# Performance work log

Measured on AMD Instinct MI355X. Metric: run time of the kernel, lower is better.

Reference implementation:

```python
import jax, jax.numpy as jnp
import numpy as np
import math

D = 512          # belief_dim
H = 128          # hidden_dim
R = 64           # relation_dim
M = 8192         # max_beliefs
N = 131072       # candidate pairs
INIT_BIAS = math.log(0.4 / 0.6) * -1.0  # = log(1.5) ~ 0.405465


def _linear_params(key, fan_in, fan_out):
    kw, kb = jax.random.split(key)
    bound = 1.0 / math.sqrt(fan_in)
    W = jax.random.uniform(kw, (fan_in, fan_out), minval=-bound, maxval=bound, dtype=jnp.float32)
    b = jax.random.uniform(kb, (fan_out,), minval=-bound, maxval=bound, dtype=jnp.float32)
    return W, b


def setup_inputs() -> dict:
    key = jax.random.key(0)
    ks = jax.random.split(key, 11)
    beliefs = jax.random.normal(ks[0], (M, D), dtype=jnp.float32)
    src_idx = jax.random.randint(ks[1], (N,), 0, M)
    tgt_idx = jax.random.randint(ks[2], (N,), 0, M)
    # proposal_net: 3D -> H -> H//2 -> 1  (last bias = log(1.5))
    pw1, pb1 = _linear_params(ks[3], 3 * D, H)
    pw2, pb2 = _linear_params(ks[4], H, H // 2)
    pw3, _ = _linear_params(ks[5], H // 2, 1)
    pb3 = jnp.full((1,), INIT_BIAS, dtype=jnp.float32)
    # direction_net: 3D -> H//2 -> 1 (sigmoid)
    dw1, db1 = _linear_params(ks[6], 3 * D, H // 2)
    dw2, db2 = _linear_params(ks[7], H // 2, 1)
    # relation_net: 3D -> H -> R
    rw1, rb1 = _linear_params(ks[8], 3 * D, H)
    rw2, rb2 = _linear_params(ks[9], H, R)
    return {
        "beliefs": beliefs, "src_idx": src_idx, "tgt_idx": tgt_idx,
        "pw1": pw1, "pb1": pb1, "pw2": pw2, "pb2": pb2, "pw3": pw3, "pb3": pb3,
        "dw1": dw1, "db1": db1, "dw2": dw2, "db2": db2,
        "rw1": rw1, "rb1": rb1, "rw2": rw2, "rb2": rb2,
    }


def reference(beliefs, src_idx, tgt_idx,
              pw1, pb1, pw2, pb2, pw3, pb3,
              dw1, db1, dw2, db2,
              rw1, rb1, rw2, rb2):
    src = beliefs[src_idx]                       # [N, D] gather
    tgt = beliefs[tgt_idx]                       # [N, D] gather
    feats = jnp.concatenate([src, tgt, jnp.abs(src - tgt)], axis=-1)  # [N, 3D]

    # proposal head -> edge probability
    h = jax.nn.relu(feats @ pw1 + pb1)
    h = jax.nn.relu(h @ pw2 + pb2)
    probs = jax.nn.sigmoid((h @ pw3 + pb3)[:, 0])                     # [N]

    # direction head -> angle in [0, pi/2]
    d = jax.nn.relu(feats @ dw1 + db1)
    directions = jax.nn.sigmoid((d @ dw2 + db2)[:, 0]) * (jnp.pi / 2)  # [N]

    # relation head -> initial relation vectors
    r = jax.nn.relu(feats @ rw1 + rb1)
    relations = r @ rw2 + rb2                                          # [N, R]

    return probs, directions, relations
```

## Files before the change

kernel.cpp:

```cpp
#include <hip/hip_runtime.h>
#include <hip/hip_bf16.h>


#define DD 512
#define K3 1536
#define ROWS 128
#define LDACT 328
#define BUFS 12288
#define BUFS2 16384

typedef short bf16x8 __attribute__((ext_vector_type(8)));
typedef float f32x4 __attribute__((ext_vector_type(4)));

__device__ inline float b2f(short s) {
    union { float f; unsigned u; } v;
    v.u = ((unsigned)(unsigned short)s) << 16;
    return v.f;
}
__device__ inline short f2b(float f) {
    union { float fl; unsigned u; } v;
    v.fl = f;
    unsigned x = v.u;
    unsigned r = x + 0x7fffu + ((x >> 16) & 1u);
    return (short)(r >> 16);
}
__device__ inline short babsdiff(short a, short b) {
    union { float f; unsigned u; } v;
    v.f = b2f(a) - b2f(b);
    return (short)((v.u & 0x7fffffffu) >> 16);
}
__device__ __forceinline__ bf16x8 babs8(bf16x8 s, bf16x8 t) {
    bf16x8 a;
#pragma unroll
    for (int j = 0; j < 8; j++) a[j] = babsdiff(s[j], t[j]);
    return a;
}

__device__ __forceinline__ int sidx32(int seg, int rt, int lane) {
    return ((seg * 8 + rt) * 64 + lane) * 8;
}
__device__ __forceinline__ void writeStage(short* buf, int rtw, int lnw, int kcb,
                                           bf16x8 s0, bf16x8 s1,
                                           bf16x8 t0, bf16x8 t1) {
    bf16x8 a0 = babs8(s0, t0), a1 = babs8(s1, t1);
    int l0 = kcb * 16 + lnw, l1 = l0 + 16;
    *(bf16x8*)&buf[sidx32(0, rtw, l0)] = s0;
    *(bf16x8*)&buf[sidx32(0, rtw, l1)] = s1;
    *(bf16x8*)&buf[sidx32(1, rtw, l0)] = t0;
    *(bf16x8*)&buf[sidx32(1, rtw, l1)] = t1;
    *(bf16x8*)&buf[sidx32(2, rtw, l0)] = a0;
    *(bf16x8*)&buf[sidx32(2, rtw, l1)] = a1;
}
__device__ __forceinline__ void stage_f32(const float* bs, const float* bt,
                                          short* buf, int rtw, int lnw, int kcb) {
#pragma unroll
    for (int c = 0; c < 2; c++) {
        bf16x8 sb, tb, ab;
#pragma unroll
        for (int h = 0; h < 2; h++) {
            float4 s4 = ((const float4*)bs)[c * 2 + h];
            float4 t4 = ((const float4*)bt)[c * 2 + h];
            float ss[4] = {s4.x, s4.y, s4.z, s4.w};
            float tt[4] = {t4.x, t4.y, t4.z, t4.w};
#pragma unroll
            for (int e = 0; e < 4; e++) {
                int j = h * 4 + e;
                sb[j] = f2b(ss[e]);
                tb[j] = f2b(tt[e]);
                ab[j] = f2b(fabsf(ss[e] - tt[e]));
            }
        }
        int l16 = (kcb + c) * 16 + lnw;
        *(bf16x8*)&buf[sidx32(0, rtw, l16)] = sb;
        *(bf16x8*)&buf[sidx32(1, rtw, l16)] = tb;
        *(bf16x8*)&buf[sidx32(2, rtw, l16)] = ab;
    }
}

#define WT_ELEMS (320 * 1536)
#define P2T_OFF WT_ELEMS
#define R2T_OFF (WT_ELEMS + 64 * 128)
#define PREP_TOT (WT_ELEMS + 2 * 64 * 128)
#define BEL_ELEMS (8192 * 512)
#define BEL_OFF PREP_TOT

__global__ void prep_kernel(const float* __restrict__ pw1,
                            const float* __restrict__ dw1,
                            const float* __restrict__ rw1,
                            const float* __restrict__ pw2,
                            const float* __restrict__ rw2,
                            const float* __restrict__ beliefs,
                            short* __restrict__ ws, int total8) {
    int i8 = blockIdx.x * 256 + threadIdx.x;
    if (i8 >= total8) return;
    int i = i8 * 8;
    bf16x8 o;
    if (i < WT_ELEMS) {
        int n = i / K3, k = i - n * K3;
        const float* src;
        int stride, off;
        if (n < 128)      { src = pw1; stride = 128; off = n; }
        else if (n < 192) { src = dw1; stride = 64;  off = n - 128; }
        else              { src = rw1; stride = 128; off = n - 192; }
#pragma unroll
        for (int j = 0; j < 8; j++) o[j] = f2b(src[(k + j) * stride + off]);
    } else if (i < R2T_OFF) {
        int jj = i - P2T_OFF;
        int n = jj >> 7, k = jj & 127;
#pragma unroll
        for (int j = 0; j < 8; j++) o[j] = f2b(pw2[(k + j) * 64 + n]);
    } else if (i < PREP_TOT) {
        int jj = i - R2T_OFF;
        int n = jj >> 7, k = jj & 127;
#pragma unroll
        for (int j = 0; j < 8; j++) o[j] = f2b(rw2[(k + j) * 64 + n]);
    } else {
        const float4* b4 = (const float4*)(beliefs + (i - BEL_OFF));
        float4 x = b4[0], y = b4[1];
        float v[8] = {x.x, x.y, x.z, x.w, y.x, y.y, y.z, y.w};
#pragma unroll
        for (int j = 0; j < 8; j++) o[j] = f2b(v[j]);
    }
    *(bf16x8*)&ws[i] = o;
}

__global__ __launch_bounds__(256) void prep_bst(
    const short* __restrict__ bel16, const short* __restrict__ WT,
    float* __restrict__ Bs, float* __restrict__ Bt) {
    const int tb = blockIdx.x & 1;
    const int r0 = (blockIdx.x >> 1) * 64;
    const int t = threadIdx.x;
    const int w = t >> 6, lane = t & 63, q = lane >> 4, ln = lane & 15;
    float* Bo = tb ? Bt : Bs;
    const int koff = tb ? 512 : 0;

    f32x4 acc[5][4];
#pragma unroll
    for (int ct = 0; ct < 5; ct++)
#pragma unroll
        for (int rt = 0; rt < 4; rt++) acc[ct][rt] = (f32x4)(0.f);

#pragma unroll
    for (int k0 = 0; k0 < 512; k0 += 128)
#pragma unroll
        for (int kk = 0; kk < 4; kk++) {
            bf16x8 bfr[5];
#pragma unroll
            for (int ct = 0; ct < 5; ct++)
                bfr[ct] = *(const bf16x8*)(WT + (size_t)(w * 80 + ct * 16 + ln) * K3 +
                                           koff + k0 + kk * 32 + q * 8);
#pragma unroll
            for (int rt = 0; rt < 4; rt++) {
                bf16x8 af = *(const bf16x8*)(bel16 +
                    (size_t)(r0 + rt * 16 + ln) * DD + k0 + kk * 32 + q * 8);
#pragma unroll
                for (int ct = 0; ct < 5; ct++)
                    acc[ct][rt] = __builtin_amdgcn_mfma_f32_16x16x32_bf16(
                        af, bfr[ct], acc[ct][rt], 0, 0, 0);
            }
        }
#pragma unroll
    for (int ct = 0; ct < 5; ct++)
#pragma unroll
        for (int rt = 0; rt < 4; rt++)
#pragma unroll
            for (int i = 0; i < 4; i++)
                Bo[(size_t)(r0 + rt * 16 + q * 4 + i) * 320 +
                   w * 80 + ct * 16 + ln] = acc[ct][rt][i];
}

__global__ __launch_bounds__(256, 2) void edge_main2(
    const short* __restrict__ bel16,
    const int* __restrict__ src_idx, const int* __restrict__ tgt_idx,
    const float* __restrict__ Bs, const float* __restrict__ Bt,
    const float* __restrict__ pb1, const float* __restrict__ db1,
    const float* __restrict__ rb1,
    const float* __restrict__ pb2, const float* __restrict__ pw3,
    const float* __restrict__ pb3,
    const float* __restrict__ dw2, const float* __restrict__ db2,
    const float* __restrict__ rb2,
    const short* __restrict__ WT, const short* __restrict__ pw2T,
    const short* __restrict__ rw2T,
    float* __restrict__ out, int N)
{
    __shared__ __align__(16) char smem_u[65536];
    __shared__ int sIdxR[ROWS], tIdxR[ROWS];
    short* As = (short*)smem_u;
    short (*acts)[LDACT] = (short (*)[LDACT])smem_u;

    const int t = threadIdx.x;
    const int r0 = blockIdx.x * ROWS;
    const int w = t >> 6, lane = t & 63, q = lane >> 4, ln = lane & 15;

    if (t < ROWS) sIdxR[t] = src_idx[r0 + t];
    else tIdxR[t - ROWS] = tgt_idx[r0 + t - ROWS];
    __syncthreads();

    const int rr = t >> 1, kh = t & 1;
    const int rtw = rr >> 4, lnw = rr & 15;
    const size_t srow = (size_t)sIdxR[rr] * DD + kh * 64;
    const size_t trow = (size_t)tIdxR[rr] * DD + kh * 64;

    f32x4 acc[5][8];
#pragma unroll
    for (int ct = 0; ct < 5; ct++)
#pragma unroll
        for (int rt = 0; rt < 8; rt++) acc[ct][rt] = (f32x4)(0.f);

#pragma unroll
    for (int c = 0; c < 8; c++) {
        bf16x8 s8 = *(const bf16x8*)(bel16 + srow + c * 8);
        bf16x8 t8 = *(const bf16x8*)(bel16 + trow + c * 8);
        bf16x8 a8 = babs8(s8, t8);
        int gg = kh * 8 + c, kd = gg >> 2, qd = gg & 3;
        *(bf16x8*)&As[((kd * 8 + rtw) * 64 + qd * 16 + lnw) * 8] = a8;
    }
    __syncthreads();

#pragma unroll
    for (int step = 0; step < 4; step++) {
        short* bufC = As + (step & 1) * BUFS2;
        short* bufN = As + ((step & 1) ^ 1) * BUFS2;
        const int k0 = step * 128;
        const bool pf = (step < 3);
        bf16x8 ps0, ps1, pt0, pt1;

#pragma unroll
        for (int kk = 0; kk < 4; kk++) {
            bf16x8 bfr[5];
#pragma unroll
            for (int ct = 0; ct < 5; ct++)
                bfr[ct] = *(const bf16x8*)(WT + (size_t)(w * 80 + ct * 16 + ln) * K3 +
                                           1024 + k0 + kk * 32 + q * 8);
            __builtin_amdgcn_sched_barrier(0);
            if (pf) {
                if (kk > 0) {
                    bf16x8 a0 = babs8(ps0, pt0), a1 = babs8(ps1, pt1);
                    int g0 = kh * 8 + 2 * (kk - 1);
                    int kd0 = g0 >> 2, qd0 = g0 & 3;
                    int g1 = g0 + 1, kd1 = g1 >> 2, qd1 = g1 & 3;
                    *(bf16x8*)&bufN[((kd0 * 8 + rtw) * 64 + qd0 * 16 + lnw) * 8] = a0;
                    *(bf16x8*)&bufN[((kd1 * 8 + rtw) * 64 + qd1 * 16 + lnw) * 8] = a1;
                }
                ps0 = *(const bf16x8*)(bel16 + srow + k0 + 128 + (2 * kk) * 8);
                ps1 = *(const bf16x8*)(bel16 + srow + k0 + 128 + (2 * kk + 1) * 8);
                pt0 = *(const bf16x8*)(bel16 + trow + k0 + 128 + (2 * kk) * 8);
                pt1 = *(const bf16x8*)(bel16 + trow + k0 + 128 + (2 * kk + 1) * 8);
            }
            __builtin_amdgcn_sched_barrier(0);
            __builtin_amdgcn_s_setprio(1);
#pragma unroll
            for (int rt = 0; rt < 8; rt++) {
                bf16x8 af = *(const bf16x8*)&bufC[((kk * 8 + rt) * 64 + lane) * 8];
#pragma unroll
                for (int ct = 0; ct < 5; ct++)
                    acc[ct][rt] = __builtin_amdgcn_mfma_f32_16x16x32_bf16(
                        af, bfr[ct], acc[ct][rt], 0, 0, 0);
            }
            __builtin_amdgcn_s_setprio(0);
        }
        if (pf) {
            bf16x8 a0 = babs8(ps0, pt0), a1 = babs8(ps1, pt1);
            int g0 = kh * 8 + 6;
            int kd0 = g0 >> 2, qd0 = g0 & 3;
            int g1 = g0 + 1, kd1 = g1 >> 2, qd1 = g1 & 3;
            *(bf16x8*)&bufN[((kd0 * 8 + rtw) * 64 + qd0 * 16 + lnw) * 8] = a0;
            *(bf16x8*)&bufN[((kd1 * 8 + rtw) * 64 + qd1 * 16 + lnw) * 8] = a1;
        }
        __syncthreads();
    }

#pragma unroll
    for (int h = 0; h < 2; h++) {
        float bias5[5];
#pragma unroll
        for (int ct = 0; ct < 5; ct++) {
            int col = w * 80 + ct * 16 + ln;
            bias5[ct] = (col < 128) ? pb1[col]
                      : (col < 192) ? db1[col - 128]
                                    : rb1[col - 192];
        }
#pragma unroll
        for (int rt4 = 0; rt4 < 4; rt4++)
#pragma unroll
            for (int i = 0; i < 4; i++) {
                int lrow = rt4 * 16 + q * 4 + i;
                const float* bsp = Bs + (size_t)sIdxR[h * 64 + lrow] * 320 +
                                   w * 80 + ln;
                const float* btp = Bt + (size_t)tIdxR[h * 64 + lrow] * 320 +
                                   w * 80 + ln;
#pragma unroll
                for (int ct = 0; ct < 5; ct++) {
                    float v = acc[ct][h * 4 + rt4][i] +
                              bsp[ct * 16] + btp[ct * 16] + bias5[ct];
                    acts[lrow][w * 80 + ct * 16 + ln] = f2b(fmaxf(v, 0.f));
                }
            }
        __syncthreads();

        {
            f32x4 rc[4];
#pragma unroll
            for (int rt = 0; rt < 4; rt++) rc[rt] = (f32x4)(0.f);
#pragma unroll
            for (int ks = 0; ks < 4; ks++) {
                bf16x8 bfr = *(const bf16x8*)(rw2T + (w * 16 + ln) * 128 +
                                              ks * 32 + q * 8);
#pragma unroll
                for (int rt = 0; rt < 4; rt++) {
                    bf16x8 afr = *(const bf16x8*)&acts[rt * 16 + ln][192 + ks * 32 + q * 8];
                    rc[rt] = __builtin_amdgcn_mfma_f32_16x16x32_bf16(afr, bfr, rc[rt], 0, 0, 0);
                }
            }
            int col = w * 16 + ln;
            float bias = rb2[col];
            float* rel = out + 2 * (size_t)N;
#pragma unroll
            for (int rt = 0; rt < 4; rt++)
#pragma unroll
                for (int i = 0; i < 4; i++) {
                    int grow = r0 + h * 64 + rt * 16 + q * 4 + i;
                    rel[(size_t)grow * 64 + col] = rc[rt][i] + bias;
                }
        }

        f32x4 pc[4];
        {
#pragma unroll
            for (int rt = 0; rt < 4; rt++) pc[rt] = (f32x4)(0.f);
#pragma unroll
            for (int ks = 0; ks < 4; ks++) {
                bf16x8 bfr = *(const bf16x8*)(pw2T + (w * 16 + ln) * 128 +
                                              ks * 32 + q * 8);
#pragma unroll
                for (int rt = 0; rt < 4; rt++) {
                    bf16x8 afr = *(const bf16x8*)&acts[rt * 16 + ln][0 + ks * 32 + q * 8];
                    pc[rt] = __builtin_amdgcn_mfma_f32_16x16x32_bf16(afr, bfr, pc[rt], 0, 0, 0);
                }
            }
        }
        __syncthreads();

        {
            int col = w * 16 + ln;
            float bias = pb2[col];
#pragma unroll
            for (int rt = 0; rt < 4; rt++)
#pragma unroll
                for (int i = 0; i < 4; i++) {
                    int lrow = rt * 16 + q * 4 + i;
                    acts[lrow][col] = f2b(fmaxf(pc[rt][i] + bias, 0.f));
                }
        }
        __syncthreads();

        if (t < 64) {
            float s = pb3[0];
#pragma unroll 8
            for (int k = 0; k < 64; k++) s += b2f(acts[t][k]) * pw3[k];
            float pr = 1.f / (1.f + __expf(-s));
            out[r0 + h * 64 + t] = pr;
        } else if (t < 128) {
            int lrow = t - 64;
            float s = db2[0];
#pragma unroll 8
            for (int k = 0; k < 64; k++) s += b2f(acts[lrow][128 + k]) * dw2[k];
            float dir = (1.f / (1.f + __expf(-s))) * 1.57079632679489662f;
            out[(size_t)N + r0 + h * 64 + lrow] = dir;
        }
        __syncthreads();
    }
}

template<bool BF>
__global__ __launch_bounds__(256, 2) void edge_main(
    const float* __restrict__ beliefs, const short* __restrict__ bel16,
    const int* __restrict__ src_idx, const int* __restrict__ tgt_idx,
    const float* __restrict__ pb1, const float* __restrict__ db1,
    const float* __restrict__ rb1,
    const float* __restrict__ pb2, const float* __restrict__ pw3,
    const float* __restrict__ pb3,
    const float* __restrict__ dw2, const float* __restrict__ db2,
    const float* __restrict__ rb2,
    const short* __restrict__ WT, const short* __restrict__ pw2T,
    const short* __restrict__ rw2T,
    float* __restrict__ out, int N)
{
    __shared__ __align__(16) char smem_u[49152];
    short* As2 = (short*)smem_u;
    short (*acts)[LDACT] = (short (*)[LDACT])smem_u;
    int* sIdx = (int*)smem_u;
    int* tIdx = sIdx + ROWS;

    const int t = threadIdx.x;
    const int r0 = blockIdx.x * ROWS;
    const int w = t >> 6, lane = t & 63, q = lane >> 4, ln = lane & 15;

    if (t < ROWS) sIdx[t] = src_idx[r0 + t] * DD;
    else tIdx[t - ROWS] = tgt_idx[r0 + t - ROWS] * DD;
    __syncthreads();

    const int rrow = t >> 1, kh = t & 1;
    const int rtw = rrow >> 4, lnw = rrow & 15;
    const int kcb = kh * 2;
    const int srow = sIdx[rrow], trow = tIdx[rrow];
    __syncthreads();

    f32x4 acc[5][8];
#pragma unroll
    for (int ct = 0; ct < 5; ct++)
#pragma unroll
        for (int rt = 0; rt < 8; rt++) acc[ct][rt] = (f32x4)(0.f);

    bf16x8 bfr0[5];
#pragma unroll
    for (int ct = 0; ct < 5; ct++) {
        int col = w * 80 + ct * 16 + ln;
        bfr0[ct] = *(const bf16x8*)(WT + (size_t)col * K3 + q * 8);
    }
    if constexpr (BF) {
        const bf16x8* pS = (const bf16x8*)(bel16 + srow + kh * 16);
        const bf16x8* pT = (const bf16x8*)(bel16 + trow + kh * 16);
        writeStage(As2, rtw, lnw, kcb, pS[0], pS[1], pT[0], pT[1]);
    } else {
        stage_f32(beliefs + srow + kh * 16, beliefs + trow + kh * 16,
                  As2, rtw, lnw, kcb);
    }
    __syncthreads();

    for (int step = 0; step < 16; ++step) {
        short* bufC = As2 + (step & 1) * BUFS;
        short* bufN = As2 + ((step & 1) ^ 1) * BUFS;
        const int k0 = step * 32;
        const bool pf = (step < 15);
        bf16x8 ns0, ns1, nt0, nt1;

#pragma unroll
        for (int seg = 0; seg < 3; seg++) {
            bf16x8 bfr[5];
            if (seg == 0) {
#pragma unroll
                for (int ct = 0; ct < 5; ct++) bfr[ct] = bfr0[ct];
            } else {
#pragma unroll
                for (int ct = 0; ct < 5; ct++) {
                    int col = w * 80 + ct * 16 + ln;
                    bfr[ct] = *(const bf16x8*)(WT + (size_t)col * K3 +
                                               seg * DD + k0 + q * 8);
                }
            }
            if (seg == 2) {
                __builtin_amdgcn_sched_barrier(0);
                if (pf) {
                    if constexpr (BF) {
                        const bf16x8* pS = (const bf16x8*)(bel16 + srow + k0 + 32 + kh * 16);
                        const bf16x8* pT = (const bf16x8*)(bel16 + trow + k0 + 32 + kh * 16);
                        ns0 = pS[0]; ns1 = pS[1]; nt0 = pT[0]; nt1 = pT[1];
                    }
#pragma unroll
                    for (int ct = 0; ct < 5; ct++) {
                        int col = w * 80 + ct * 16 + ln;
                        bfr0[ct] = *(const bf16x8*)(WT + (size_t)col * K3 +
                                                    k0 + 32 + q * 8);
                    }
                }
                __builtin_amdgcn_sched_barrier(0);
            }
            __builtin_amdgcn_s_setprio(1);
#pragma unroll
            for (int rt = 0; rt < 8; rt++) {
                bf16x8 af = *(const bf16x8*)&bufC[sidx32(seg, rt, lane)];
#pragma unroll
                for (int ct = 0; ct < 5; ct++)
                    acc[ct][rt] = __builtin_amdgcn_mfma_f32_16x16x32_bf16(
                        af, bfr[ct], acc[ct][rt], 0, 0, 0);
            }
            __builtin_amdgcn_s_setprio(0);
        }
        if constexpr (BF) {
            if (pf) writeStage(bufN, rtw, lnw, kcb, ns0, ns1, nt0, nt1);
        } else {
            if (pf) stage_f32(beliefs + srow + k0 + 32 + kh * 16,
                              beliefs + trow + k0 + 32 + kh * 16,
                              bufN, rtw, lnw, kcb);
        }
        __syncthreads();
    }

#pragma unroll
    for (int h = 0; h < 2; h++) {
#pragma unroll
        for (int ct = 0; ct < 5; ct++) {
            int col = w * 80 + ct * 16 + ln;
            float bias = (col < 128) ? pb1[col]
                       : (col < 192) ? db1[col - 128]
                                     : rb1[col - 192];
#pragma unroll
            for (int rt4 = 0; rt4 < 4; rt4++)
#pragma unroll
                for (int i = 0; i < 4; i++) {
                    int lrow = rt4 * 16 + q * 4 + i;
                    float v = acc[ct][h * 4 + rt4][i] + bias;
                    acts[lrow][col] = f2b(fmaxf(v, 0.f));
                }
        }
        __syncthreads();
        {
            f32x4 rc[4];
#pragma unroll
            for (int rt = 0; rt < 4; rt++) rc[rt] = (f32x4)(0.f);
#pragma unroll
            for (int ks = 0; ks < 4; ks++) {
                bf16x8 bfr = *(const bf16x8*)(rw2T + (w * 16 + ln) * 128 +
                                              ks * 32 + q * 8);
#pragma unroll
                for (int rt = 0; rt < 4; rt++) {
                    bf16x8 afr = *(const bf16x8*)&acts[rt * 16 + ln][192 + ks * 32 + q * 8];
                    rc[rt] = __builtin_amdgcn_mfma_f32_16x16x32_bf16(afr, bfr, rc[rt], 0, 0, 0);
                }
            }
            int col = w * 16 + ln;
            float bias = rb2[col];
            float* rel = out + 2 * (size_t)N;
#pragma unroll
            for (int rt = 0; rt < 4; rt++)
#pragma unroll
                for (int i = 0; i < 4; i++) {
                    int grow = r0 + h * 64 + rt * 16 + q * 4 + i;
                    rel[(size_t)grow * 64 + col] = rc[rt][i] + bias;
                }
        }
        f32x4 pc[4];
        {
#pragma unroll
            for (int rt = 0; rt < 4; rt++) pc[rt] = (f32x4)(0.f);
#pragma unroll
            for (int ks = 0; ks < 4; ks++) {
                bf16x8 bfr = *(const bf16x8*)(pw2T + (w * 16 + ln) * 128 +
                                              ks * 32 + q * 8);
#pragma unroll
                for (int rt = 0; rt < 4; rt++) {
                    bf16x8 afr = *(const bf16x8*)&acts[rt * 16 + ln][0 + ks * 32 + q * 8];
                    pc[rt] = __builtin_amdgcn_mfma_f32_16x16x32_bf16(afr, bfr, pc[rt], 0, 0, 0);
                }
            }
        }
        __syncthreads();
        {
            int col = w * 16 + ln;
            float bias = pb2[col];
#pragma unroll
            for (int rt = 0; rt < 4; rt++)
#pragma unroll
                for (int i = 0; i < 4; i++) {
                    int lrow = rt * 16 + q * 4 + i;
                    acts[lrow][col] = f2b(fmaxf(pc[rt][i] + bias, 0.f));
                }
        }
        __syncthreads();
        if (t < 64) {
            float s = pb3[0];
#pragma unroll 8
            for (int k = 0; k < 64; k++) s += b2f(acts[t][k]) * pw3[k];
            float pr = 1.f / (1.f + __expf(-s));
            out[r0 + h * 64 + t] = pr;
        } else if (t < 128) {
            int lrow = t - 64;
            float s = db2[0];
#pragma unroll 8
            for (int k = 0; k < 64; k++) s += b2f(acts[lrow][128 + k]) * dw2[k];
            float dir = (1.f / (1.f + __expf(-s))) * 1.57079632679489662f;
            out[(size_t)N + r0 + h * 64 + lrow] = dir;
        }
        __syncthreads();
    }
}

extern "C" void kernel_launch(void* const* d_in, const int* in_sizes, int n_in,
                              void* d_out, int out_size, void* d_ws, size_t ws_size,
                              hipStream_t stream) {
    const float* beliefs = (const float*)d_in[0];
    const int* src = (const int*)d_in[1];
    const int* tgt = (const int*)d_in[2];
    const float* pw1 = (const float*)d_in[3];
    const float* pb1 = (const float*)d_in[4];
    const float* pw2 = (const float*)d_in[5];
    const float* pb2 = (const float*)d_in[6];
    const float* pw3 = (const float*)d_in[7];
    const float* pb3 = (const float*)d_in[8];
    const float* dw1 = (const float*)d_in[9];
    const float* db1 = (const float*)d_in[10];
    const float* dw2 = (const float*)d_in[11];
    const float* db2 = (const float*)d_in[12];
    const float* rw1 = (const float*)d_in[13];
    const float* rb1 = (const float*)d_in[14];
    const float* rw2 = (const float*)d_in[15];
    const float* rb2 = (const float*)d_in[16];

    short* ws = (short*)d_ws;
    short* WT    = ws;
    short* pw2T  = ws + P2T_OFF;
    short* rw2T  = ws + R2T_OFF;
    short* bel16 = ws + BEL_OFF;
    const int N = in_sizes[1];

    const size_t BF_BYTES = (size_t)(PREP_TOT + BEL_ELEMS) * sizeof(short);
    const size_t FULL_BYTES = BF_BYTES + (size_t)2 * 8192 * 320 * sizeof(float);
    const bool useV2 = ws_size >= FULL_BYTES;
    const bool useBf = ws_size >= BF_BYTES;
    const int prepElems = useBf ? (PREP_TOT + BEL_ELEMS) : PREP_TOT;
    const int prep8 = prepElems / 8;

    prep_kernel<<<(prep8 + 255) / 256, 256, 0, stream>>>(
        pw1, dw1, rw1, pw2, rw2, beliefs, ws, prep8);

    if (useV2) {
        float* Bsp = (float*)(ws + PREP_TOT + BEL_ELEMS);
        float* Btp = Bsp + (size_t)8192 * 320;
        prep_bst<<<256, 256, 0, stream>>>(bel16, WT, Bsp, Btp);
        edge_main2<<<N / ROWS, 256, 0, stream>>>(
            bel16, src, tgt, Bsp, Btp,
            pb1, db1, rb1, pb2, pw3, pb3, dw2, db2, rb2,
            WT, pw2T, rw2T, (float*)d_out, N);
    } else if (useBf) {
        edge_main<true><<<N / ROWS, 256, 0, stream>>>(
            beliefs, bel16, src, tgt, pb1, db1, rb1, pb2, pw3, pb3,
            dw2, db2, rb2, WT, pw2T, rw2T, (float*)d_out, N);
    } else {
        edge_main<false><<<N / ROWS, 256, 0, stream>>>(
            beliefs, bel16, src, tgt, pb1, db1, rb1, pb2, pw3, pb3,
            dw2, db2, rb2, WT, pw2T, rw2T, (float*)d_out, N);
    }
}
```

Baseline: 251.4 us.

## Halve edge tile to 64 rows for higher occupancy and parallelize output heads

The main edge kernel now processes 64 rows per block instead of 128. Shared memory drops to 32KB, accumulators to 5x4, and launch bounds rise to 3 blocks per CU, so more waves are resident to hide gather latency. The precompute kernel also launches twice as many blocks with smaller row tiles. The final proposal/direction dot products are split across 4 lanes with shuffle reductions, so all 256 threads work instead of 128. The trade-off is that weight fragments are reloaded per block across twice as many blocks, and each MFMA tile gets less reuse.

```diff
diff --git a/kernel.cpp b/kernel.cpp
--- a/kernel.cpp
+++ b/kernel.cpp
@@ -5,9 +5,11 @@
 #define DD 512
 #define K3 1536
 #define ROWS 128
+#define RB3 64
 #define LDACT 328
 #define BUFS 12288
 #define BUFS2 16384
+#define BUFS3 8192
 
 typedef short bf16x8 __attribute__((ext_vector_type(8)));
 typedef float f32x4 __attribute__((ext_vector_type(4)));
@@ -128,17 +130,17 @@
     const short* __restrict__ bel16, const short* __restrict__ WT,
     float* __restrict__ Bs, float* __restrict__ Bt) {
     const int tb = blockIdx.x & 1;
-    const int r0 = (blockIdx.x >> 1) * 64;
+    const int r0 = (blockIdx.x >> 1) * 32;
     const int t = threadIdx.x;
     const int w = t >> 6, lane = t & 63, q = lane >> 4, ln = lane & 15;
     float* Bo = tb ? Bt : Bs;
     const int koff = tb ? 512 : 0;
 
-    f32x4 acc[5][4];
+    f32x4 acc[5][2];
 #pragma unroll
     for (int ct = 0; ct < 5; ct++)
 #pragma unroll
-        for (int rt = 0; rt < 4; rt++) acc[ct][rt] = (f32x4)(0.f);
+        for (int rt = 0; rt < 2; rt++) acc[ct][rt] = (f32x4)(0.f);
 
 #pragma unroll
     for (int k0 = 0; k0 < 512; k0 += 128)
@@ -150,7 +152,7 @@
                 bfr[ct] = *(const bf16x8*)(WT + (size_t)(w * 80 + ct * 16 + ln) * K3 +
                                            koff + k0 + kk * 32 + q * 8);
 #pragma unroll
-            for (int rt = 0; rt < 4; rt++) {
+            for (int rt = 0; rt < 2; rt++) {
                 bf16x8 af = *(const bf16x8*)(bel16 +
                     (size_t)(r0 + rt * 16 + ln) * DD + k0 + kk * 32 + q * 8);
 #pragma unroll
@@ -162,14 +164,14 @@
 #pragma unroll
     for (int ct = 0; ct < 5; ct++)
 #pragma unroll
-        for (int rt = 0; rt < 4; rt++)
+        for (int rt = 0; rt < 2; rt++)
 #pragma unroll
             for (int i = 0; i < 4; i++)
                 Bo[(size_t)(r0 + rt * 16 + q * 4 + i) * 320 +
                    w * 80 + ct * 16 + ln] = acc[ct][rt][i];
 }
 
-__global__ __launch_bounds__(256, 2) void edge_main2(
+__global__ __launch_bounds__(256, 3) void edge_main3(
     const short* __restrict__ bel16,
     const int* __restrict__ src_idx, const int* __restrict__ tgt_idx,
     const float* __restrict__ Bs, const float* __restrict__ Bt,
@@ -183,47 +185,46 @@
     const short* __restrict__ rw2T,
     float* __restrict__ out, int N)
 {
-    __shared__ __align__(16) char smem_u[65536];
-    __shared__ int sIdxR[ROWS], tIdxR[ROWS];
+    __shared__ __align__(16) char smem_u[32768];
+    __shared__ int sIdxR[RB3], tIdxR[RB3];
     short* As = (short*)smem_u;
     short (*acts)[LDACT] = (short (*)[LDACT])smem_u;
 
     const int t = threadIdx.x;
-    const int r0 = blockIdx.x * ROWS;
+    const int r0 = blockIdx.x * RB3;
     const int w = t >> 6, lane = t & 63, q = lane >> 4, ln = lane & 15;
 
-    if (t < ROWS) sIdxR[t] = src_idx[r0 + t];
-    else tIdxR[t - ROWS] = tgt_idx[r0 + t - ROWS];
+    if (t < RB3) sIdxR[t] = src_idx[r0 + t];
+    else if (t < 2 * RB3) tIdxR[t - RB3] = tgt_idx[r0 + t - RB3];
     __syncthreads();
 
-    const int rr = t >> 1, kh = t & 1;
+    const int rr = t >> 2, cc = t & 3;
     const int rtw = rr >> 4, lnw = rr & 15;
-    const size_t srow = (size_t)sIdxR[rr] * DD + kh * 64;
-    const size_t trow = (size_t)tIdxR[rr] * DD + kh * 64;
-
-    f32x4 acc[5][8];
+    const size_t srow = (size_t)sIdxR[rr] * DD;
+    const size_t trow = (size_t)tIdxR[rr] * DD;
+
+    f32x4 acc[5][4];
 #pragma unroll
     for (int ct = 0; ct < 5; ct++)
 #pragma unroll
-        for (int rt = 0; rt < 8; rt++) acc[ct][rt] = (f32x4)(0.f);
-
-#pragma unroll
-    for (int c = 0; c < 8; c++) {
-        bf16x8 s8 = *(const bf16x8*)(bel16 + srow + c * 8);
-        bf16x8 t8 = *(const bf16x8*)(bel16 + trow + c * 8);
+        for (int rt = 0; rt < 4; rt++) acc[ct][rt] = (f32x4)(0.f);
+
+#pragma unroll
+    for (int qd = 0; qd < 4; qd++) {
+        bf16x8 s8 = *(const bf16x8*)(bel16 + srow + cc * 32 + qd * 8);
+        bf16x8 t8 = *(const bf16x8*)(bel16 + trow + cc * 32 + qd * 8);
         bf16x8 a8 = babs8(s8, t8);
-        int gg = kh * 8 + c, kd = gg >> 2, qd = gg & 3;
-        *(bf16x8*)&As[((kd * 8 + rtw) * 64 + qd * 16 + lnw) * 8] = a8;
+        *(bf16x8*)&As[((cc * 4 + rtw) * 64 + qd * 16 + lnw) * 8] = a8;
     }
     __syncthreads();
 
 #pragma unroll
     for (int step = 0; step < 4; step++) {
-        short* bufC = As + (step & 1) * BUFS2;
-        short* bufN = As + ((step & 1) ^ 1) * BUFS2;
+        short* bufC = As + (step & 1) * BUFS3;
+        short* bufN = As + ((step & 1) ^ 1) * BUFS3;
         const int k0 = step * 128;
         const bool pf = (step < 3);
-        bf16x8 ps0, ps1, pt0, pt1;
+        bf16x8 ps, pt;
 
 #pragma unroll
         for (int kk = 0; kk < 4; kk++) {
@@ -235,23 +236,17 @@
             __builtin_amdgcn_sched_barrier(0);
             if (pf) {
                 if (kk > 0) {
-                    bf16x8 a0 = babs8(ps0, pt0), a1 = babs8(ps1, pt1);
-                    int g0 = kh * 8 + 2 * (kk - 1);
-                    int kd0 = g0 >> 2, qd0 = g0 & 3;
-                    int g1 = g0 + 1, kd1 = g1 >> 2, qd1 = g1 & 3;
-                    *(bf16x8*)&bufN[((kd0 * 8 + rtw) * 64 + qd0 * 16 + lnw) * 8] = a0;
-                    *(bf16x8*)&bufN[((kd1 * 8 + rtw) * 64 + qd1 * 16 + lnw) * 8] = a1;
-                }
-                ps0 = *(const bf16x8*)(bel16 + srow + k0 + 128 + (2 * kk) * 8);
-                ps1 = *(const bf16x8*)(bel16 + srow + k0 + 128 + (2 * kk + 1) * 8);
-                pt0 = *(const bf16x8*)(bel16 + trow + k0 + 128 + (2 * kk) * 8);
-                pt1 = *(const bf16x8*)(bel16 + trow + k0 + 128 + (2 * kk + 1) * 8);
+                    bf16x8 a8 = babs8(ps, pt);
+                    *(bf16x8*)&bufN[((cc * 4 + rtw) * 64 + (kk - 1) * 16 + lnw) * 8] = a8;
+                }
+                ps = *(const bf16x8*)(bel16 + srow + k0 + 128 + cc * 32 + kk * 8);
+                pt = *(const bf16x8*)(bel16 + trow + k0 + 128 + cc * 32 + kk * 8);
             }
             __builtin_amdgcn_sched_barrier(0);
             __builtin_amdgcn_s_setprio(1);
 #pragma unroll
-            for (int rt = 0; rt < 8; rt++) {
-                bf16x8 af = *(const bf16x8*)&bufC[((kk * 8 + rt) * 64 + lane) * 8];
+            for (int rt = 0; rt < 4; rt++) {
+                bf16x8 af = *(const bf16x8*)&bufC[((kk * 4 + rt) * 64 + lane) * 8];
 #pragma unroll
                 for (int ct = 0; ct < 5; ct++)
                     acc[ct][rt] = __builtin_amdgcn_mfma_f32_16x16x32_bf16(
@@ -260,18 +255,14 @@
             __builtin_amdgcn_s_setprio(0);
         }
         if (pf) {
-            bf16x8 a0 = babs8(ps0, pt0), a1 = babs8(ps1, pt1);
-            int g0 = kh * 8 + 6;
-            int kd0 = g0 >> 2, qd0 = g0 & 3;
-            int g1 = g0 + 1, kd1 = g1 >> 2, qd1 = g1 & 3;
-            *(bf16x8*)&bufN[((kd0 * 8 + rtw) * 64 + qd0 * 16 + lnw) * 8] = a0;
-            *(bf16x8*)&bufN[((kd1 * 8 + rtw) * 64 + qd1 * 16 + lnw) * 8] = a1;
-        }
-        __syncthreads();
-    }
-
-#pragma unroll
-    for (int h = 0; h < 2; h++) {
+            bf16x8 a8 = babs8(ps, pt);
+            *(bf16x8*)&bufN[((cc * 4 + rtw) * 64 + 3 * 16 + lnw) * 8] = a8;
+        }
+        __syncthreads();
+    }
+
+#pragma unroll
+    for (int hh = 0; hh < 2; hh++) {
         float bias5[5];
 #pragma unroll
         for (int ct = 0; ct < 5; ct++) {
@@ -281,17 +272,17 @@
                                     : rb1[col - 192];
         }
 #pragma unroll
-        for (int rt4 = 0; rt4 < 4; rt4++)
+        for (int rt2 = 0; rt2 < 2; rt2++)
 #pragma unroll
             for (int i = 0; i < 4; i++) {
-                int lrow = rt4 * 16 + q * 4 + i;
-                const float* bsp = Bs + (size_t)sIdxR[h * 64 + lrow] * 320 +
+                int lrow = rt2 * 16 + q * 4 + i;
+                const float* bsp = Bs + (size_t)sIdxR[hh * 32 + lrow] * 320 +
                                    w * 80 + ln;
-                const float* btp = Bt + (size_t)tIdxR[h * 64 + lrow] * 320 +
+                const float* btp = Bt + (size_t)tIdxR[hh * 32 + lrow] * 320 +
                                    w * 80 + ln;
 #pragma unroll
                 for (int ct = 0; ct < 5; ct++) {
-                    float v = acc[ct][h * 4 + rt4][i] +
+                    float v = acc[ct][hh * 2 + rt2][i] +
                               bsp[ct * 16] + btp[ct * 16] + bias5[ct];
                     acts[lrow][w * 80 + ct * 16 + ln] = f2b(fmaxf(v, 0.f));
                 }
@@ -299,43 +290,43 @@
         __syncthreads();
 
         {
-            f32x4 rc[4];
-#pragma unroll
-            for (int rt = 0; rt < 4; rt++) rc[rt] = (f32x4)(0.f);
+            f32x4 rc[2];
+#pragma unroll
+            for (int rt2 = 0; rt2 < 2; rt2++) rc[rt2] = (f32x4)(0.f);
 #pragma unroll
             for (int ks = 0; ks < 4; ks++) {
                 bf16x8 bfr = *(const bf16x8*)(rw2T + (w * 16 + ln) * 128 +
                                               ks * 32 + q * 8);
 #pragma unroll
-                for (int rt = 0; rt < 4; rt++) {
-                    bf16x8 afr = *(const bf16x8*)&acts[rt * 16 + ln][192 + ks * 32 + q * 8];
-                    rc[rt] = __builtin_amdgcn_mfma_f32_16x16x32_bf16(afr, bfr, rc[rt], 0, 0, 0);
+                for (int rt2 = 0; rt2 < 2; rt2++) {
+                    bf16x8 afr = *(const bf16x8*)&acts[rt2 * 16 + ln][192 + ks * 32 + q * 8];
+                    rc[rt2] = __builtin_amdgcn_mfma_f32_16x16x32_bf16(afr, bfr, rc[rt2], 0, 0, 0);
                 }
             }
             int col = w * 16 + ln;
             float bias = rb2[col];
             float* rel = out + 2 * (size_t)N;
 #pragma unroll
-            for (int rt = 0; rt < 4; rt++)
+            for (int rt2 = 0; rt2 < 2; rt2++)
 #pragma unroll
                 for (int i = 0; i < 4; i++) {
-                    int grow = r0 + h * 64 + rt * 16 + q * 4 + i;
-                    rel[(size_t)grow * 64 + col] = rc[rt][i] + bias;
-                }
-        }
-
-        f32x4 pc[4];
+                    int grow = r0 + hh * 32 + rt2 * 16 + q * 4 + i;
+                    rel[(size_t)grow * 64 + col] = rc[rt2][i] + bias;
+                }
+        }
+
+        f32x4 pc[2];
         {
 #pragma unroll
-            for (int rt = 0; rt < 4; rt++) pc[rt] = (f32x4)(0.f);
+            for (int rt2 = 0; rt2 < 2; rt2++) pc[rt2] = (f32x4)(0.f);
 #pragma unroll
             for (int ks = 0; ks < 4; ks++) {
                 bf16x8 bfr = *(const bf16x8*)(pw2T + (w * 16 + ln) * 128 +
                                               ks * 32 + q * 8);
 #pragma unroll
-                for (int rt = 0; rt < 4; rt++) {
-                    bf16x8 afr = *(const bf16x8*)&acts[rt * 16 + ln][0 + ks * 32 + q * 8];
-                    pc[rt] = __builtin_amdgcn_mfma_f32_16x16x32_bf16(afr, bfr, pc[rt], 0, 0, 0);
+                for (int rt2 = 0; rt2 < 2; rt2++) {
+                    bf16x8 afr = *(const bf16x8*)&acts[rt2 * 16 + ln][0 + ks * 32 + q * 8];
+                    pc[rt2] = __builtin_amdgcn_mfma_f32_16x16x32_bf16(afr, bfr, pc[rt2], 0, 0, 0);
                 }
             }
         }
@@ -345,28 +336,41 @@
             int col = w * 16 + ln;
             float bias = pb2[col];
 #pragma unroll
-            for (int rt = 0; rt < 4; rt++)
+            for (int rt2 = 0; rt2 < 2; rt2++)
 #pragma unroll
                 for (int i = 0; i < 4; i++) {
-                    int lrow = rt * 16 + q * 4 + i;
-                    acts[lrow][col] = f2b(fmaxf(pc[rt][i] + bias, 0.f));
-                }
-        }
-        __syncthreads();
-
-        if (t < 64) {
-            float s = pb3[0];
-#pragma unroll 8
-            for (int k = 0; k < 64; k++) s += b2f(acts[t][k]) * pw3[k];
-            float pr = 1.f / (1.f + __expf(-s));
-            out[r0 + h * 64 + t] = pr;
-        } else if (t < 128) {
-            int lrow = t - 64;
-            float s = db2[0];
-#pragma unroll 8
-            for (int k = 0; k < 64; k++) s += b2f(acts[lrow][128 + k]) * dw2[k];
-            float dir = (1.f / (1.f + __expf(-s))) * 1.57079632679489662f;
-            out[(size_t)N + r0 + h * 64 + lrow] = dir;
+                    int lrow = rt2 * 16 + q * 4 + i;
+                    acts[lrow][col] = f2b(fmaxf(pc[rt2][i] + bias, 0.f));
+                }
+        }
+        __syncthreads();
+
+        {
+            int role = t >> 7;
+            int rloc = (t & 127) >> 2;
+            int kq = t & 3;
+            float s = 0.f;
+            if (role == 0) {
+#pragma unroll
+                for (int j = 0; j < 16; j++)
+                    s += b2f(acts[rloc][kq * 16 + j]) * pw3[kq * 16 + j];
+            } else {
+#pragma unroll
+                for (int j = 0; j < 16; j++)
+                    s += b2f(acts[rloc][128 + kq * 16 + j]) * dw2[kq * 16 + j];
+            }
+            s += __shfl_xor(s, 1);
+            s += __shfl_xor(s, 2);
+            if (kq == 0) {
+                if (role == 0) {
+                    float pr = 1.f / (1.f + __expf(-(s + pb3[0])));
+                    out[r0 + hh * 32 + rloc] = pr;
+                } else {
+                    float dir = (1.f / (1.f + __expf(-(s + db2[0])))) *
+                                1.57079632679489662f;
+                    out[(size_t)N + r0 + hh * 32 + rloc] = dir;
+                }
+            }
         }
         __syncthreads();
     }
@@ -617,8 +621,8 @@
     if (useV2) {
         float* Bsp = (float*)(ws + PREP_TOT + BEL_ELEMS);
         float* Btp = Bsp + (size_t)8192 * 320;
-        prep_bst<<<256, 256, 0, stream>>>(bel16, WT, Bsp, Btp);
-        edge_main2<<<N / ROWS, 256, 0, stream>>>(
+        prep_bst<<<512, 256, 0, stream>>>(bel16, WT, Bsp, Btp);
+        edge_main3<<<N / RB3, 256, 0, stream>>>(
             bel16, src, tgt, Bsp, Btp,
             pb1, db1, rb1, pb2, pw3, pb3, dw2, db2, rb2,
             WT, pw2T, rw2T, (float*)d_out, N);
```

New measurement: 271.3 us. +7.9%, slower.

## Store per-belief partial projections as packed bf16 and fuse belief conversion

Applied to the files above, without the earlier changes.

The precomputed per-belief projections of the src and tgt feature slices are now stored as bf16 in a packed layout: 5 values per lane, padded to 8 shorts. Each edge row can then gather its partial sums with one 16-byte load instead of ten scattered fp32 loads, which cuts gather bandwidth in the main kernel. The bf16 conversion of beliefs moves out of the prep kernel into the projection kernel, which now reads fp32 beliefs directly and runs with smaller row tiles across more blocks. The final proposal and direction dot products are also split across 256 threads with a shuffle reduction. Rounding the partial sums to bf16 adds some precision loss.

```diff
diff --git a/kernel.cpp b/kernel.cpp
--- a/kernel.cpp
+++ b/kernel.cpp
@@ -83,6 +83,7 @@
 #define PREP_TOT (WT_ELEMS + 2 * 64 * 128)
 #define BEL_ELEMS (8192 * 512)
 #define BEL_OFF PREP_TOT
+#define TBL_ELEMS (8192 * 4 * 16 * 8)
 
 __global__ void prep_kernel(const float* __restrict__ pw1,
                             const float* __restrict__ dw1,
@@ -124,21 +125,22 @@
     *(bf16x8*)&ws[i] = o;
 }
 
-__global__ __launch_bounds__(256) void prep_bst(
-    const short* __restrict__ bel16, const short* __restrict__ WT,
-    float* __restrict__ Bs, float* __restrict__ Bt) {
+__global__ __launch_bounds__(256) void prep_bst2(
+    const float* __restrict__ beliefs, const short* __restrict__ WT,
+    short* __restrict__ BsT, short* __restrict__ BtT,
+    short* __restrict__ bel16) {
     const int tb = blockIdx.x & 1;
-    const int r0 = (blockIdx.x >> 1) * 64;
+    const int r0 = (blockIdx.x >> 1) * 32;
     const int t = threadIdx.x;
     const int w = t >> 6, lane = t & 63, q = lane >> 4, ln = lane & 15;
-    float* Bo = tb ? Bt : Bs;
+    short* Bo = tb ? BtT : BsT;
     const int koff = tb ? 512 : 0;
 
-    f32x4 acc[5][4];
+    f32x4 acc[5][2];
 #pragma unroll
     for (int ct = 0; ct < 5; ct++)
 #pragma unroll
-        for (int rt = 0; rt < 4; rt++) acc[ct][rt] = (f32x4)(0.f);
+        for (int rt = 0; rt < 2; rt++) acc[ct][rt] = (f32x4)(0.f);
 
 #pragma unroll
     for (int k0 = 0; k0 < 512; k0 += 128)
@@ -150,9 +152,14 @@
                 bfr[ct] = *(const bf16x8*)(WT + (size_t)(w * 80 + ct * 16 + ln) * K3 +
                                            koff + k0 + kk * 32 + q * 8);
 #pragma unroll
-            for (int rt = 0; rt < 4; rt++) {
-                bf16x8 af = *(const bf16x8*)(bel16 +
+            for (int rt = 0; rt < 2; rt++) {
+                const float4* ap = (const float4*)(beliefs +
                     (size_t)(r0 + rt * 16 + ln) * DD + k0 + kk * 32 + q * 8);
+                float4 a0 = ap[0], a1 = ap[1];
+                float av[8] = {a0.x, a0.y, a0.z, a0.w, a1.x, a1.y, a1.z, a1.w};
+                bf16x8 af;
+#pragma unroll
+                for (int j = 0; j < 8; j++) af[j] = f2b(av[j]);
 #pragma unroll
                 for (int ct = 0; ct < 5; ct++)
                     acc[ct][rt] = __builtin_amdgcn_mfma_f32_16x16x32_bf16(
@@ -160,19 +167,36 @@
             }
         }
 #pragma unroll
-    for (int ct = 0; ct < 5; ct++)
-#pragma unroll
-        for (int rt = 0; rt < 4; rt++)
-#pragma unroll
-            for (int i = 0; i < 4; i++)
-                Bo[(size_t)(r0 + rt * 16 + q * 4 + i) * 320 +
-                   w * 80 + ct * 16 + ln] = acc[ct][rt][i];
+    for (int rt = 0; rt < 2; rt++)
+#pragma unroll
+        for (int i = 0; i < 4; i++) {
+            int r = r0 + rt * 16 + q * 4 + i;
+            size_t base = ((size_t)(r * 4 + w) * 16 + ln) * 8;
+#pragma unroll
+            for (int ct = 0; ct < 5; ct++)
+                Bo[base + ct] = f2b(acc[ct][rt][i]);
+        }
+    if (tb == 0) {
+#pragma unroll
+        for (int j = 0; j < 8; j++) {
+            int c = t * 8 + j;
+            int row = c >> 6, k8 = (c & 63) * 8;
+            const float4* bp = (const float4*)(beliefs +
+                (size_t)(r0 + row) * DD + k8);
+            float4 x = bp[0], y = bp[1];
+            float v[8] = {x.x, x.y, x.z, x.w, y.x, y.y, y.z, y.w};
+            bf16x8 o;
+#pragma unroll
+            for (int e = 0; e < 8; e++) o[e] = f2b(v[e]);
+            *(bf16x8*)&bel16[(size_t)(r0 + row) * DD + k8] = o;
+        }
+    }
 }
 
 __global__ __launch_bounds__(256, 2) void edge_main2(
     const short* __restrict__ bel16,
     const int* __restrict__ src_idx, const int* __restrict__ tgt_idx,
-    const float* __restrict__ Bs, const float* __restrict__ Bt,
+    const short* __restrict__ BsT, const short* __restrict__ BtT,
     const float* __restrict__ pb1, const float* __restrict__ db1,
     const float* __restrict__ rb1,
     const float* __restrict__ pb2, const float* __restrict__ pw3,
@@ -271,7 +295,7 @@
     }
 
 #pragma unroll
-    for (int h = 0; h < 2; h++) {
+    for (int hh = 0; hh < 2; hh++) {
         float bias5[5];
 #pragma unroll
         for (int ct = 0; ct < 5; ct++) {
@@ -281,21 +305,27 @@
                                     : rb1[col - 192];
         }
 #pragma unroll
-        for (int rt4 = 0; rt4 < 4; rt4++)
+        for (int rt4 = 0; rt4 < 4; rt4++) {
+            bf16x8 bs8[4], bt8[4];
+#pragma unroll
+            for (int i = 0; i < 4; i++) {
+                int gr = hh * 64 + rt4 * 16 + q * 4 + i;
+                bs8[i] = *(const bf16x8*)(BsT +
+                    ((size_t)(sIdxR[gr] * 4 + w) * 16 + ln) * 8);
+                bt8[i] = *(const bf16x8*)(BtT +
+                    ((size_t)(tIdxR[gr] * 4 + w) * 16 + ln) * 8);
+            }
 #pragma unroll
             for (int i = 0; i < 4; i++) {
                 int lrow = rt4 * 16 + q * 4 + i;
-                const float* bsp = Bs + (size_t)sIdxR[h * 64 + lrow] * 320 +
-                                   w * 80 + ln;
-                const float* btp = Bt + (size_t)tIdxR[h * 64 + lrow] * 320 +
-                                   w * 80 + ln;
 #pragma unroll
                 for (int ct = 0; ct < 5; ct++) {
-                    float v = acc[ct][h * 4 + rt4][i] +
-                              bsp[ct * 16] + btp[ct * 16] + bias5[ct];
+                    float v = acc[ct][hh * 4 + rt4][i] +
+                              b2f(bs8[i][ct]) + b2f(bt8[i][ct]) + bias5[ct];
                     acts[lrow][w * 80 + ct * 16 + ln] = f2b(fmaxf(v, 0.f));
                 }
             }
+        }
         __syncthreads();
 
         {
@@ -319,7 +349,7 @@
             for (int rt = 0; rt < 4; rt++)
 #pragma unroll
                 for (int i = 0; i < 4; i++) {
-                    int grow = r0 + h * 64 + rt * 16 + q * 4 + i;
+                    int grow = r0 + hh * 64 + rt * 16 + q * 4 + i;
                     rel[(size_t)grow * 64 + col] = rc[rt][i] + bias;
                 }
         }
@@ -354,19 +384,31 @@
         }
         __syncthreads();
 
-        if (t < 64) {
-            float s = pb3[0];
-#pragma unroll 8
-            for (int k = 0; k < 64; k++) s += b2f(acts[t][k]) * pw3[k];
-            float pr = 1.f / (1.f + __expf(-s));
-            out[r0 + h * 64 + t] = pr;
-        } else if (t < 128) {
-            int lrow = t - 64;
-            float s = db2[0];
-#pragma unroll 8
-            for (int k = 0; k < 64; k++) s += b2f(acts[lrow][128 + k]) * dw2[k];
-            float dir = (1.f / (1.f + __expf(-s))) * 1.57079632679489662f;
-            out[(size_t)N + r0 + h * 64 + lrow] = dir;
+        {
+            int role = t >> 7;
+            int rloc = (t & 127) >> 1;
+            int kq = t & 1;
+            float s = 0.f;
+            if (role == 0) {
+#pragma unroll
+                for (int j = 0; j < 32; j++)
+                    s += b2f(acts[rloc][kq * 32 + j]) * pw3[kq * 32 + j];
+            } else {
+#pragma unroll
+                for (int j = 0; j < 32; j++)
+                    s += b2f(acts[rloc][128 + kq * 32 + j]) * dw2[kq * 32 + j];
+            }
+            s += __shfl_xor(s, 1);
+            if (kq == 0) {
+                if (role == 0) {
+                    float pr = 1.f / (1.f + __expf(-(s + pb3[0])));
+                    out[r0 + hh * 64 + rloc] = pr;
+                } else {
+                    float dir = (1.f / (1.f + __expf(-(s + db2[0])))) *
+                                1.57079632679489662f;
+                    out[(size_t)N + r0 + hh * 64 + rloc] = dir;
+                }
+            }
         }
         __syncthreads();
     }
@@ -605,30 +647,33 @@
     const int N = in_sizes[1];
 
     const size_t BF_BYTES = (size_t)(PREP_TOT + BEL_ELEMS) * sizeof(short);
-    const size_t FULL_BYTES = BF_BYTES + (size_t)2 * 8192 * 320 * sizeof(float);
-    const bool useV2 = ws_size >= FULL_BYTES;
+    const size_t V2_BYTES = BF_BYTES + (size_t)2 * TBL_ELEMS * sizeof(short);
+    const bool useV2 = ws_size >= V2_BYTES;
     const bool useBf = ws_size >= BF_BYTES;
-    const int prepElems = useBf ? (PREP_TOT + BEL_ELEMS) : PREP_TOT;
-    const int prep8 = prepElems / 8;
-
-    prep_kernel<<<(prep8 + 255) / 256, 256, 0, stream>>>(
-        pw1, dw1, rw1, pw2, rw2, beliefs, ws, prep8);
 
     if (useV2) {
-        float* Bsp = (float*)(ws + PREP_TOT + BEL_ELEMS);
-        float* Btp = Bsp + (size_t)8192 * 320;
-        prep_bst<<<256, 256, 0, stream>>>(bel16, WT, Bsp, Btp);
+        const int prep8 = PREP_TOT / 8;
+        prep_kernel<<<(prep8 + 255) / 256, 256, 0, stream>>>(
+            pw1, dw1, rw1, pw2, rw2, beliefs, ws, prep8);
+        short* BsT = ws + PREP_TOT + BEL_ELEMS;
+        short* BtT = BsT + TBL_ELEMS;
+        prep_bst2<<<512, 256, 0, stream>>>(beliefs, WT, BsT, BtT, bel16);
         edge_main2<<<N / ROWS, 256, 0, stream>>>(
-            bel16, src, tgt, Bsp, Btp,
+            bel16, src, tgt, BsT, BtT,
             pb1, db1, rb1, pb2, pw3, pb3, dw2, db2, rb2,
             WT, pw2T, rw2T, (float*)d_out, N);
-    } else if (useBf) {
-        edge_main<true><<<N / ROWS, 256, 0, stream>>>(
-            beliefs, bel16, src, tgt, pb1, db1, rb1, pb2, pw3, pb3,
-            dw2, db2, rb2, WT, pw2T, rw2T, (float*)d_out, N);
     } else {
-        edge_main<false><<<N / ROWS, 256, 0, stream>>>(
-            beliefs, bel16, src, tgt, pb1, db1, rb1, pb2, pw3, pb3,
-            dw2, db2, rb2, WT, pw2T, rw2T, (float*)d_out, N);
-    }
-}
+        const int prepElems = useBf ? (PREP_TOT + BEL_ELEMS) : PREP_TOT;
+        const int prep8 = prepElems / 8;
+        prep_kernel<<<(prep8 + 255) / 256, 256, 0, stream>>>(
+            pw1, dw1, rw1, pw2, rw2, beliefs, ws, prep8);
+        if (useBf)
+            edge_main<true><<<N / ROWS, 256, 0, stream>>>(
+                beliefs, bel16, src, tgt, pb1, db1, rb1, pb2, pw3, pb3,
+                dw2, db2, rb2, WT, pw2T, rw2T, (float*)d_out, N);
+        else
+            edge_main<false><<<N / ROWS, 256, 0, stream>>>(
+                beliefs, bel16, src, tgt, pb1, db1, rb1, pb2, pw3, pb3,
+                dw2, db2, rb2, WT, pw2T, rw2T, (float*)d_out, N);
+    }
+}
```

After: 268.5 us. +6.8%, slower.
